# Kernel tuning notes

Measured on AMD Instinct MI355X. Metric: run time of the kernel, lower is better.

## Reference

```python
import jax, jax.numpy as jnp
import numpy as np
import math

DIM = 4096
N_HEADS = 32
HEAD_DIM = DIM // N_HEADS  # 128
SEQLEN = 2048


def setup_inputs() -> dict:
    key = jax.random.key(0)
    ks = jax.random.split(key, 8)
    x = jax.random.normal(ks[0], (1, SEQLEN, DIM), dtype=jnp.float32)
    # freqs_cis as real view: (seqlen, head_dim//2, 2) = (cos, sin) of rotary angles
    theta = 10000.0 ** (-jnp.arange(0, HEAD_DIM, 2, dtype=jnp.float32) / HEAD_DIM)
    angles = jnp.arange(SEQLEN, dtype=jnp.float32)[:, None] * theta[None, :]
    freqs = jnp.stack([jnp.cos(angles), jnp.sin(angles)], axis=-1)  # (S, 64, 2)
    # causal additive mask (use -1e9 instead of -inf for numeric safety)
    mask = jnp.triu(jnp.full((SEQLEN, SEQLEN), -1e9, dtype=jnp.float32), k=1)[None, None]
    scale = 1.0 / math.sqrt(DIM)
    wq = jax.random.normal(ks[1], (DIM, DIM), dtype=jnp.float32) * scale
    wk = jax.random.normal(ks[2], (DIM, DIM), dtype=jnp.float32) * scale
    wv = jax.random.normal(ks[3], (DIM, DIM), dtype=jnp.float32) * scale
    wo = jax.random.normal(ks[4], (DIM, DIM), dtype=jnp.float32) * scale
    return {"x": x, "start_pos": 0, "freqs": freqs, "mask": mask,
            "wq": wq, "wk": wk, "wv": wv, "wo": wo}


def _rotary(xq, xk, freqs, seqlen, n_heads, head_dim):
    # Faithful to source: note the repo's slice(0, 2) means xq_ == xq (no pair swap).
    ll = freqs[:, :, 0:1]  # (S, hd/2, 1) cos
    rr = freqs[:, :, 1:2]  # (S, hd/2, 1) sin
    fl = jnp.concatenate([ll, ll], axis=-1).reshape(seqlen, 1, head_dim)
    fr = jnp.concatenate([-rr, rr], axis=-1).reshape(seqlen, 1, head_dim)
    xq_ = xq.reshape(seqlen, n_heads, head_dim // 2, 2).reshape(seqlen, n_heads, head_dim)  # == xq
    xk_ = xk.reshape(seqlen, n_heads, head_dim // 2, 2).reshape(seqlen, n_heads, head_dim)  # == xk
    return xq * fl + xq_ * fr, xk * fl + xk_ * fr


def reference(x, start_pos, freqs, mask, wq, wk, wv, wo):
    bsz, seqlen, dim = x.shape  # bsz == 1 (source squeezes batch)
    xs = x[0]  # (S, D) -- HE encrypt/linear/decrypt roundtrip == plain linear
    xq = xs @ wq.T
    xk = xs @ wk.T
    xv = xs @ wv.T
    xq = xq.reshape(seqlen, N_HEADS, HEAD_DIM)
    xk = xk.reshape(seqlen, N_HEADS, HEAD_DIM)
    xv = xv.reshape(seqlen, N_HEADS, HEAD_DIM)
    xq, xk = _rotary(xq, xk, freqs, seqlen, N_HEADS, HEAD_DIM)
    # start_pos == 0 and zero-initialized cache => keys/values are just xk/xv
    q = jnp.transpose(xq, (1, 0, 2))  # (H, S, Dh)
    k = jnp.transpose(xk, (1, 0, 2))
    v = jnp.transpose(xv, (1, 0, 2))
    scores = jnp.einsum('hqd,hkd->hqk', q, k) / math.sqrt(HEAD_DIM)  # (H, S, S)
    scores = scores[None] + mask  # (1, H, S, S)
    probs = jax.nn.softmax(scores, axis=-1)
    out = jnp.einsum('bhqk,hkd->bhqd', probs, v)  # (1, H, S, Dh)
    out = jnp.transpose(out, (0, 2, 1, 3)).reshape(bsz, seqlen, dim)
    return out @ wo.T
```

## Files before the change

kernel.cpp:

```cpp
#include <hip/hip_runtime.h>

#define DIM 4096
#define SEQ 2048
#define NH 32
#define HD 128

typedef __bf16 bf16x8 __attribute__((ext_vector_type(8)));
typedef float f32x4 __attribute__((ext_vector_type(4)));

#define QSCALE 0.12751649736765598f

__device__ inline ushort f2bf(float f) {
    union { float f; unsigned u; } v; v.f = f;
    unsigned r = v.u + 0x7fffu + ((v.u >> 16) & 1u);
    return (ushort)(r >> 16);
}

__global__ void conv_all(const float* __restrict__ x,  const float* __restrict__ wq,
                         const float* __restrict__ wk, const float* __restrict__ wv,
                         const float* __restrict__ wo,
                         ushort* __restrict__ xb,  ushort* __restrict__ wqb,
                         ushort* __restrict__ wkb, ushort* __restrict__ wvb,
                         ushort* __restrict__ wob) {
    int i = blockIdx.x * 256 + threadIdx.x;
    const float* src; ushort* dst; int off;
    const int n4x = (SEQ * DIM) / 4;
    if (i < n4x) { src = x; dst = xb; off = i; }
    else {
        int j = i - n4x;
        int w = j >> 22;
        off = j & ((1 << 22) - 1);
        src = (w == 0) ? wq : (w == 1) ? wk : (w == 2) ? wv : wo;
        dst = (w == 0) ? wqb : (w == 1) ? wkb : (w == 2) ? wvb : wob;
    }
    float4 v = ((const float4*)src)[off];
    ushort4 o;
    o.x = f2bf(v.x); o.y = f2bf(v.y); o.z = f2bf(v.z); o.w = f2bf(v.w);
    ((ushort4*)dst)[off] = o;
}

__global__ __launch_bounds__(256)
void gemm_qkv(const ushort* __restrict__ A,
              const ushort* __restrict__ Bq, const ushort* __restrict__ Bk,
              const ushort* __restrict__ Bv,
              ushort* __restrict__ qout, ushort* __restrict__ kout,
              ushort* __restrict__ vt, const float* __restrict__ freqs) {
    __shared__ __align__(16) ushort sA[128 * 32];
    __shared__ __align__(16) ushort sB[128 * 32];
    const int bi = blockIdx.x;
    const int jj = bi >> 3;
    const int mblk = (bi & 7) * 2 + (jj & 1);
    const int nblk = jj >> 1;
    const int wsel = nblk >> 5;
    const int nloc = (nblk & 31) * 128;
    const int m0 = mblk * 128;
    const int tid = threadIdx.x;
    const int wave = tid >> 6, lane = tid & 63;
    const int quad = lane >> 4, c = lane & 15;
    const int wm = (wave >> 1) * 64, wn = (wave & 1) * 64;
    const ushort* B = (wsel == 0) ? Bq : (wsel == 1) ? Bk : Bv;
    const int K = DIM;

    const f32x4 vzero = {0.f, 0.f, 0.f, 0.f};
    f32x4 acc[4][4];
#pragma unroll
    for (int i = 0; i < 4; i++)
#pragma unroll
        for (int j = 0; j < 4; j++) acc[i][j] = vzero;

    const int srow = lane >> 2;
    const int sg   = ((lane & 3) - (srow >> 1)) & 3;
    const int scol = sg * 8;
    const int rpos = (quad + ((c >> 1) & 3)) & 3;
    const size_t arow0 = (size_t)(m0 + wave * 32) * K;
    const size_t brow0 = (size_t)(nloc + wave * 32) * K;

    for (int k0 = 0; k0 < K; k0 += 32) {
#pragma unroll
        for (int j = 0; j < 2; j++) {
            __builtin_amdgcn_global_load_lds(
                (const __attribute__((address_space(1))) void*)(A + arow0 + (size_t)(j * 16 + srow) * K + k0 + scol),
                (__attribute__((address_space(3))) void*)(&sA[(wave * 32 + j * 16) * 32]), 16, 0, 0);
            __builtin_amdgcn_global_load_lds(
                (const __attribute__((address_space(1))) void*)(B + brow0 + (size_t)(j * 16 + srow) * K + k0 + scol),
                (__attribute__((address_space(3))) void*)(&sB[(wave * 32 + j * 16) * 32]), 16, 0, 0);
        }
        __syncthreads();
        bf16x8 af[4], bfr[4];
#pragma unroll
        for (int t = 0; t < 4; t++) {
            af[t]  = *(const bf16x8*)&sA[(wm + t * 16 + c) * 32 + rpos * 8];
            bfr[t] = *(const bf16x8*)&sB[(wn + t * 16 + c) * 32 + rpos * 8];
        }
#pragma unroll
        for (int mt = 0; mt < 4; mt++)
#pragma unroll
            for (int nt = 0; nt < 4; nt++)
                acc[mt][nt] = __builtin_amdgcn_mfma_f32_16x16x32_bf16(af[mt], bfr[nt], acc[mt][nt], 0, 0, 0);
        __syncthreads();
    }

    if (wsel < 2) {
        ushort* Cw = wsel ? kout : qout;
        const float qs = wsel ? 1.0f : QSCALE;
#pragma unroll
        for (int mt = 0; mt < 4; mt++) {
#pragma unroll
            for (int nt = 0; nt < 4; nt++) {
                int colg = nloc + wn + nt * 16 + c;
                int dh = (colg & 127) >> 1;
#pragma unroll
                for (int r = 0; r < 4; r++) {
                    int row = m0 + wm + mt * 16 + quad * 4 + r;
                    float2 f2 = ((const float2*)freqs)[row * 64 + dh];
                    float f = (f2.x + ((c & 1) ? f2.y : -f2.y)) * qs;
                    Cw[(size_t)row * DIM + colg] = f2bf(acc[mt][nt][r] * f);
                }
            }
        }
    } else {
#pragma unroll
        for (int mt = 0; mt < 4; mt++) {
#pragma unroll
            for (int nt = 0; nt < 4; nt++) {
                int cv = nloc + wn + nt * 16 + c;
                int row0 = m0 + wm + mt * 16 + quad * 4;
                ushort4 o;
                o.x = f2bf(acc[mt][nt][0]); o.y = f2bf(acc[mt][nt][1]);
                o.z = f2bf(acc[mt][nt][2]); o.w = f2bf(acc[mt][nt][3]);
                *(ushort4*)&vt[(size_t)cv * SEQ + row0] = o;
            }
        }
    }
}

__global__ __launch_bounds__(256)
void gemm_f32out(const ushort* __restrict__ A, const ushort* __restrict__ B,
                 float* __restrict__ C, int M, int N, int K) {
    __shared__ __align__(16) ushort sA[128 * 32];
    __shared__ __align__(16) ushort sB[128 * 32];
    const int bi = blockIdx.x;
    const int jj = bi >> 3;
    const int mblk = (bi & 7) * 2 + (jj & 1);
    const int nblk = jj >> 1;
    const int m0 = mblk * 128, n0 = nblk * 128;
    const int tid = threadIdx.x;
    const int wave = tid >> 6, lane = tid & 63;
    const int quad = lane >> 4, c = lane & 15;
    const int wm = (wave >> 1) * 64, wn = (wave & 1) * 64;

    const f32x4 vzero = {0.f, 0.f, 0.f, 0.f};
    f32x4 acc[4][4];
#pragma unroll
    for (int i = 0; i < 4; i++)
#pragma unroll
        for (int j = 0; j < 4; j++) acc[i][j] = vzero;

    const int srow = lane >> 2;
    const int sg   = ((lane & 3) - (srow >> 1)) & 3;
    const int scol = sg * 8;
    const int rpos = (quad + ((c >> 1) & 3)) & 3;
    const size_t arow0 = (size_t)(m0 + wave * 32) * K;
    const size_t brow0 = (size_t)(n0 + wave * 32) * K;

    for (int k0 = 0; k0 < K; k0 += 32) {
#pragma unroll
        for (int j = 0; j < 2; j++) {
            __builtin_amdgcn_global_load_lds(
                (const __attribute__((address_space(1))) void*)(A + arow0 + (size_t)(j * 16 + srow) * K + k0 + scol),
                (__attribute__((address_space(3))) void*)(&sA[(wave * 32 + j * 16) * 32]), 16, 0, 0);
            __builtin_amdgcn_global_load_lds(
                (const __attribute__((address_space(1))) void*)(B + brow0 + (size_t)(j * 16 + srow) * K + k0 + scol),
                (__attribute__((address_space(3))) void*)(&sB[(wave * 32 + j * 16) * 32]), 16, 0, 0);
        }
        __syncthreads();
        bf16x8 af[4], bfr[4];
#pragma unroll
        for (int t = 0; t < 4; t++) {
            af[t]  = *(const bf16x8*)&sA[(wm + t * 16 + c) * 32 + rpos * 8];
            bfr[t] = *(const bf16x8*)&sB[(wn + t * 16 + c) * 32 + rpos * 8];
        }
#pragma unroll
        for (int mt = 0; mt < 4; mt++)
#pragma unroll
            for (int nt = 0; nt < 4; nt++)
                acc[mt][nt] = __builtin_amdgcn_mfma_f32_16x16x32_bf16(af[mt], bfr[nt], acc[mt][nt], 0, 0, 0);
        __syncthreads();
    }

#pragma unroll
    for (int mt = 0; mt < 4; mt++)
#pragma unroll
        for (int nt = 0; nt < 4; nt++)
#pragma unroll
            for (int r = 0; r < 4; r++) {
                int row = m0 + wm + mt * 16 + quad * 4 + r;
                int col = n0 + wn + nt * 16 + c;
                C[(size_t)row * N + col] = acc[mt][nt][r];
            }
}

__global__ __launch_bounds__(256)
void flash_kernel(const ushort* __restrict__ Q, const ushort* __restrict__ K,
                  const ushort* __restrict__ Vt, ushort* __restrict__ O) {
    const int bi = blockIdx.x;
    const int h = bi & (NH - 1);
    const int p = bi >> 5;
    __shared__ __align__(16) ushort sK[64 * 128];
    __shared__ __align__(16) ushort sVt[128 * 64];
    __shared__ __align__(16) ushort sP[4][16 * 72];
    const int tid = threadIdx.x, wave = tid >> 6, lane = tid & 63;
    const int quad = lane >> 4, c = lane & 15;

    for (int pass = 0; pass < 2; pass++) {
        const int qb = pass ? (SEQ / 64 - 1 - p) : p;
        const int q0 = qb * 64;

        bf16x8 qf[4];
        {
            const ushort* Qp = Q + (size_t)(q0 + wave * 16 + c) * DIM + h * HD;
#pragma unroll
            for (int ks = 0; ks < 4; ks++) qf[ks] = *(const bf16x8*)(Qp + ks * 32 + quad * 8);
        }
        const f32x4 vzero = {0.f, 0.f, 0.f, 0.f};
        f32x4 oa[8];
#pragma unroll
        for (int dt = 0; dt < 8; dt++) oa[dt] = vzero;
        float ms[4], ls[4];
#pragma unroll
        for (int r = 0; r < 4; r++) { ms[r] = -1e30f; ls[r] = 0.f; }

        for (int kt = 0; kt <= qb; kt++) {
            __syncthreads();
#pragma unroll
            for (int i = 0; i < 4; i++) {
                int lr = wave * 16 + i * 4 + (lane >> 4);
                int ch = lane & 15;
                int g = (ch & 8) | ((ch ^ lr) & 7);
                __builtin_amdgcn_global_load_lds(
                    (const __attribute__((address_space(1))) void*)(K + (size_t)(kt * 64 + lr) * DIM + h * HD + g * 8),
                    (__attribute__((address_space(3))) void*)(&sK[(wave * 16 + i * 4) * 128]), 16, 0, 0);
            }
#pragma unroll
            for (int i = 0; i < 4; i++) {
                int ld = wave * 32 + i * 8 + (lane >> 3);
                int ch = lane & 7;
                int g = (ch ^ ld) & 7;
                __builtin_amdgcn_global_load_lds(
                    (const __attribute__((address_space(1))) void*)(Vt + (size_t)(h * HD + ld) * SEQ + kt * 64 + g * 8),
                    (__attribute__((address_space(3))) void*)(&sVt[(wave * 32 + i * 8) * 64]), 16, 0, 0);
            }
            __syncthreads();

            f32x4 s[4];
#pragma unroll
            for (int nt = 0; nt < 4; nt++) s[nt] = vzero;
#pragma unroll
            for (int ks = 0; ks < 4; ks++)
#pragma unroll
                for (int nt = 0; nt < 4; nt++) {
                    int lr = nt * 16 + c;
                    int gc = ks * 4 + quad;
                    int pch = (gc & 8) | ((gc ^ lr) & 7);
                    bf16x8 kf = *(const bf16x8*)&sK[lr * 128 + pch * 8];
                    s[nt] = __builtin_amdgcn_mfma_f32_16x16x32_bf16(qf[ks], kf, s[nt], 0, 0, 0);
                }

            if (kt == qb) {
#pragma unroll
                for (int nt = 0; nt < 4; nt++)
#pragma unroll
                    for (int r = 0; r < 4; r++) {
                        int keyg = nt * 16 + c;
                        int qg   = wave * 16 + quad * 4 + r;
                        if (keyg > qg) s[nt][r] = -1e30f;
                    }
            }

            float mnew[4], alpha[4];
#pragma unroll
            for (int r = 0; r < 4; r++) {
                float v = fmaxf(fmaxf(s[0][r], s[1][r]), fmaxf(s[2][r], s[3][r]));
                v = fmaxf(v, __shfl_xor(v, 1));
                v = fmaxf(v, __shfl_xor(v, 2));
                v = fmaxf(v, __shfl_xor(v, 4));
                v = fmaxf(v, __shfl_xor(v, 8));
                mnew[r]  = fmaxf(ms[r], v);
                alpha[r] = exp2f(ms[r] - mnew[r]);
                ms[r]    = mnew[r];
            }
            float rs[4] = {0.f, 0.f, 0.f, 0.f};
#pragma unroll
            for (int nt = 0; nt < 4; nt++)
#pragma unroll
                for (int r = 0; r < 4; r++) {
                    float pv = exp2f(s[nt][r] - mnew[r]);
                    rs[r] += pv;
                    sP[wave][(quad * 4 + r) * 72 + nt * 16 + c] = f2bf(pv);
                }
#pragma unroll
            for (int r = 0; r < 4; r++) {
                float v = rs[r];
                v += __shfl_xor(v, 1);
                v += __shfl_xor(v, 2);
                v += __shfl_xor(v, 4);
                v += __shfl_xor(v, 8);
                ls[r] = ls[r] * alpha[r] + v;
            }
#pragma unroll
            for (int dt = 0; dt < 8; dt++)
#pragma unroll
                for (int r = 0; r < 4; r++) oa[dt][r] *= alpha[r];

            __asm__ volatile("s_waitcnt lgkmcnt(0)" ::: "memory");

#pragma unroll
            for (int k2 = 0; k2 < 2; k2++) {
                bf16x8 pf = *(const bf16x8*)&sP[wave][c * 72 + k2 * 32 + quad * 8];
#pragma unroll
                for (int dt = 0; dt < 8; dt++) {
                    int ld = dt * 16 + c;
                    int gc = k2 * 4 + quad;
                    int pch = (gc ^ ld) & 7;
                    bf16x8 vf = *(const bf16x8*)&sVt[ld * 64 + pch * 8];
                    oa[dt] = __builtin_amdgcn_mfma_f32_16x16x32_bf16(pf, vf, oa[dt], 0, 0, 0);
                }
            }
        }

#pragma unroll
        for (int r = 0; r < 4; r++) {
            float inv = 1.f / ls[r];
            int row = q0 + wave * 16 + quad * 4 + r;
#pragma unroll
            for (int dt = 0; dt < 8; dt++)
                O[(size_t)row * DIM + h * HD + dt * 16 + c] = f2bf(oa[dt][r] * inv);
        }
    }
}

extern "C" void kernel_launch(void* const* d_in, const int* in_sizes, int n_in,
                              void* d_out, int out_size, void* d_ws, size_t ws_size,
                              hipStream_t stream) {
    const float* x     = (const float*)d_in[0];
    const float* freqs = (const float*)d_in[2];
    const float* wq    = (const float*)d_in[4];
    const float* wk    = (const float*)d_in[5];
    const float* wv    = (const float*)d_in[6];
    const float* wo    = (const float*)d_in[7];
    float* out = (float*)d_out;

    ushort* xb    = (ushort*)d_ws;
    ushort* wqb   = xb    + (size_t)SEQ * DIM;
    ushort* wkb   = wqb   + (size_t)DIM * DIM;
    ushort* wvb   = wkb   + (size_t)DIM * DIM;
    ushort* wob   = wvb   + (size_t)DIM * DIM;
    ushort* qbuf  = wob   + (size_t)DIM * DIM;
    ushort* kbuf  = qbuf  + (size_t)SEQ * DIM;
    ushort* vtbuf = kbuf  + (size_t)SEQ * DIM;
    ushort* obuf  = vtbuf + (size_t)SEQ * DIM;

    const int n4tot = (SEQ * DIM + 4 * DIM * DIM) / 4;
    conv_all<<<n4tot / 256, 256, 0, stream>>>(x, wq, wk, wv, wo, xb, wqb, wkb, wvb, wob);

    gemm_qkv<<<dim3(3 * DIM / 128 * SEQ / 128), 256, 0, stream>>>(
        xb, wqb, wkb, wvb, qbuf, kbuf, vtbuf, freqs);

    flash_kernel<<<dim3(NH * SEQ / 128), 256, 0, stream>>>(qbuf, kbuf, vtbuf, obuf);

    gemm_f32out<<<dim3(DIM / 128 * SEQ / 128), 256, 0, stream>>>(obuf, wob, out, SEQ, DIM, DIM);
}
```

Baseline: 804.8 us.

## Double K-tile depth to 64 with XOR swizzle and remap block-to-tile order

Both GEMM kernels now stage 64-wide K slices in LDS instead of 32. This halves the number of barrier pairs per output tile and puts two MFMA sub-steps between syncs. The LDS layout switches to an 8-way XOR swizzle to avoid bank conflicts at the wider row. Block index mapping is also reordered so that the blocks sharing an XCD (bi&7) cover contiguous N-tiles across all M, aiming for better L2 reuse of weights. LDS use doubles to 32KB per block, which may lower occupancy.

Result: faster. 765.0 us (-4.9%).

```diff
diff --git a/kernel.cpp b/kernel.cpp
--- a/kernel.cpp
+++ b/kernel.cpp
@@ -45,12 +45,13 @@
               const ushort* __restrict__ Bv,
               ushort* __restrict__ qout, ushort* __restrict__ kout,
               ushort* __restrict__ vt, const float* __restrict__ freqs) {
-    __shared__ __align__(16) ushort sA[128 * 32];
-    __shared__ __align__(16) ushort sB[128 * 32];
+    __shared__ __align__(16) ushort sA[128 * 64];
+    __shared__ __align__(16) ushort sB[128 * 64];
     const int bi = blockIdx.x;
-    const int jj = bi >> 3;
-    const int mblk = (bi & 7) * 2 + (jj & 1);
-    const int nblk = jj >> 1;
+    const int x = bi & 7;
+    const int l = bi >> 3;
+    const int mblk = l & 15;
+    const int nblk = x * 12 + (l >> 4);
     const int wsel = nblk >> 5;
     const int nloc = (nblk & 31) * 128;
     const int m0 = mblk * 128;
@@ -68,35 +69,40 @@
 #pragma unroll
         for (int j = 0; j < 4; j++) acc[i][j] = vzero;
 
-    const int srow = lane >> 2;
-    const int sg   = ((lane & 3) - (srow >> 1)) & 3;
-    const int scol = sg * 8;
-    const int rpos = (quad + ((c >> 1) & 3)) & 3;
+    const int srow8 = lane >> 3;
+    const int sg    = (lane & 7) ^ srow8;
+    const int scol  = sg * 8;
+    const int rp0 = ((0 * 4 + quad) ^ (c & 7)) * 8;
+    const int rp1 = ((1 * 4 + quad) ^ (c & 7)) * 8;
     const size_t arow0 = (size_t)(m0 + wave * 32) * K;
     const size_t brow0 = (size_t)(nloc + wave * 32) * K;
 
-    for (int k0 = 0; k0 < K; k0 += 32) {
-#pragma unroll
-        for (int j = 0; j < 2; j++) {
+    for (int k0 = 0; k0 < K; k0 += 64) {
+#pragma unroll
+        for (int i = 0; i < 4; i++) {
             __builtin_amdgcn_global_load_lds(
-                (const __attribute__((address_space(1))) void*)(A + arow0 + (size_t)(j * 16 + srow) * K + k0 + scol),
-                (__attribute__((address_space(3))) void*)(&sA[(wave * 32 + j * 16) * 32]), 16, 0, 0);
+                (const __attribute__((address_space(1))) void*)(A + arow0 + (size_t)(i * 8 + srow8) * K + k0 + scol),
+                (__attribute__((address_space(3))) void*)(&sA[(wave * 32 + i * 8) * 64]), 16, 0, 0);
             __builtin_amdgcn_global_load_lds(
-                (const __attribute__((address_space(1))) void*)(B + brow0 + (size_t)(j * 16 + srow) * K + k0 + scol),
-                (__attribute__((address_space(3))) void*)(&sB[(wave * 32 + j * 16) * 32]), 16, 0, 0);
+                (const __attribute__((address_space(1))) void*)(B + brow0 + (size_t)(i * 8 + srow8) * K + k0 + scol),
+                (__attribute__((address_space(3))) void*)(&sB[(wave * 32 + i * 8) * 64]), 16, 0, 0);
         }
         __syncthreads();
-        bf16x8 af[4], bfr[4];
-#pragma unroll
-        for (int t = 0; t < 4; t++) {
-            af[t]  = *(const bf16x8*)&sA[(wm + t * 16 + c) * 32 + rpos * 8];
-            bfr[t] = *(const bf16x8*)&sB[(wn + t * 16 + c) * 32 + rpos * 8];
-        }
-#pragma unroll
-        for (int mt = 0; mt < 4; mt++)
-#pragma unroll
-            for (int nt = 0; nt < 4; nt++)
-                acc[mt][nt] = __builtin_amdgcn_mfma_f32_16x16x32_bf16(af[mt], bfr[nt], acc[mt][nt], 0, 0, 0);
+#pragma unroll
+        for (int kk = 0; kk < 2; kk++) {
+            const int rp = kk ? rp1 : rp0;
+            bf16x8 af[4], bfr[4];
+#pragma unroll
+            for (int t = 0; t < 4; t++) {
+                af[t]  = *(const bf16x8*)&sA[(wm + t * 16 + c) * 64 + rp];
+                bfr[t] = *(const bf16x8*)&sB[(wn + t * 16 + c) * 64 + rp];
+            }
+#pragma unroll
+            for (int mt = 0; mt < 4; mt++)
+#pragma unroll
+                for (int nt = 0; nt < 4; nt++)
+                    acc[mt][nt] = __builtin_amdgcn_mfma_f32_16x16x32_bf16(af[mt], bfr[nt], acc[mt][nt], 0, 0, 0);
+        }
         __syncthreads();
     }
 
@@ -137,12 +143,13 @@
 __global__ __launch_bounds__(256)
 void gemm_f32out(const ushort* __restrict__ A, const ushort* __restrict__ B,
                  float* __restrict__ C, int M, int N, int K) {
-    __shared__ __align__(16) ushort sA[128 * 32];
-    __shared__ __align__(16) ushort sB[128 * 32];
+    __shared__ __align__(16) ushort sA[128 * 64];
+    __shared__ __align__(16) ushort sB[128 * 64];
     const int bi = blockIdx.x;
-    const int jj = bi >> 3;
-    const int mblk = (bi & 7) * 2 + (jj & 1);
-    const int nblk = jj >> 1;
+    const int x = bi & 7;
+    const int l = bi >> 3;
+    const int mblk = l & 15;
+    const int nblk = x * 4 + (l >> 4);
     const int m0 = mblk * 128, n0 = nblk * 128;
     const int tid = threadIdx.x;
     const int wave = tid >> 6, lane = tid & 63;
@@ -156,35 +163,40 @@
 #pragma unroll
         for (int j = 0; j < 4; j++) acc[i][j] = vzero;
 
-    const int srow = lane >> 2;
-    const int sg   = ((lane & 3) - (srow >> 1)) & 3;
-    const int scol = sg * 8;
-    const int rpos = (quad + ((c >> 1) & 3)) & 3;
+    const int srow8 = lane >> 3;
+    const int sg    = (lane & 7) ^ srow8;
+    const int scol  = sg * 8;
+    const int rp0 = ((0 * 4 + quad) ^ (c & 7)) * 8;
+    const int rp1 = ((1 * 4 + quad) ^ (c & 7)) * 8;
     const size_t arow0 = (size_t)(m0 + wave * 32) * K;
     const size_t brow0 = (size_t)(n0 + wave * 32) * K;
 
-    for (int k0 = 0; k0 < K; k0 += 32) {
-#pragma unroll
-        for (int j = 0; j < 2; j++) {
+    for (int k0 = 0; k0 < K; k0 += 64) {
+#pragma unroll
+        for (int i = 0; i < 4; i++) {
             __builtin_amdgcn_global_load_lds(
-                (const __attribute__((address_space(1))) void*)(A + arow0 + (size_t)(j * 16 + srow) * K + k0 + scol),
-                (__attribute__((address_space(3))) void*)(&sA[(wave * 32 + j * 16) * 32]), 16, 0, 0);
+                (const __attribute__((address_space(1))) void*)(A + arow0 + (size_t)(i * 8 + srow8) * K + k0 + scol),
+                (__attribute__((address_space(3))) void*)(&sA[(wave * 32 + i * 8) * 64]), 16, 0, 0);
             __builtin_amdgcn_global_load_lds(
-                (const __attribute__((address_space(1))) void*)(B + brow0 + (size_t)(j * 16 + srow) * K + k0 + scol),
-                (__attribute__((address_space(3))) void*)(&sB[(wave * 32 + j * 16) * 32]), 16, 0, 0);
+                (const __attribute__((address_space(1))) void*)(B + brow0 + (size_t)(i * 8 + srow8) * K + k0 + scol),
+                (__attribute__((address_space(3))) void*)(&sB[(wave * 32 + i * 8) * 64]), 16, 0, 0);
         }
         __syncthreads();
-        bf16x8 af[4], bfr[4];
-#pragma unroll
-        for (int t = 0; t < 4; t++) {
-            af[t]  = *(const bf16x8*)&sA[(wm + t * 16 + c) * 32 + rpos * 8];
-            bfr[t] = *(const bf16x8*)&sB[(wn + t * 16 + c) * 32 + rpos * 8];
-        }
-#pragma unroll
-        for (int mt = 0; mt < 4; mt++)
-#pragma unroll
-            for (int nt = 0; nt < 4; nt++)
-                acc[mt][nt] = __builtin_amdgcn_mfma_f32_16x16x32_bf16(af[mt], bfr[nt], acc[mt][nt], 0, 0, 0);
+#pragma unroll
+        for (int kk = 0; kk < 2; kk++) {
+            const int rp = kk ? rp1 : rp0;
+            bf16x8 af[4], bfr[4];
+#pragma unroll
+            for (int t = 0; t < 4; t++) {
+                af[t]  = *(const bf16x8*)&sA[(wm + t * 16 + c) * 64 + rp];
+                bfr[t] = *(const bf16x8*)&sB[(wn + t * 16 + c) * 64 + rp];
+            }
+#pragma unroll
+            for (int mt = 0; mt < 4; mt++)
+#pragma unroll
+                for (int nt = 0; nt < 4; nt++)
+                    acc[mt][nt] = __builtin_amdgcn_mfma_f32_16x16x32_bf16(af[mt], bfr[nt], acc[mt][nt], 0, 0, 0);
+        }
         __syncthreads();
     }
 
```
